# Optimization experiments

Hardware: AMD Instinct MI355X
Metric: run time of the kernel (lower is better)

## Reference

```python
import jax, jax.numpy as jnp
import numpy as np

B, S, I, H, O = 64, 512, 1024, 1024, 1024


def setup_inputs() -> dict:
    key = jax.random.key(0)
    ks = jax.random.split(key, 10)
    s = 0.02
    return {
        "x": jax.random.normal(ks[0], (B, S, I), dtype=jnp.float32),
        "W_hi": jax.random.normal(ks[1], (H, H), dtype=jnp.float32) * s,
        "W_ii": jax.random.normal(ks[2], (I, H), dtype=jnp.float32) * s,
        "W_hf": jax.random.normal(ks[3], (H, H), dtype=jnp.float32) * s,
        "W_if": jax.random.normal(ks[4], (I, H), dtype=jnp.float32) * s,
        "W_ho": jax.random.normal(ks[5], (H, H), dtype=jnp.float32) * s,
        "W_io": jax.random.normal(ks[6], (I, H), dtype=jnp.float32) * s,
        "W_hg": jax.random.normal(ks[7], (H, H), dtype=jnp.float32) * s,
        "W_ig": jax.random.normal(ks[8], (I, H), dtype=jnp.float32) * s,
        "W_y": jax.random.normal(ks[9], (H, O), dtype=jnp.float32) * s,
    }


def reference(x, W_hi, W_ii, W_hf, W_if, W_ho, W_io, W_hg, W_ig, W_y):
    b = x.shape[0]
    h0 = jnp.zeros((b, W_hi.shape[0]), dtype=x.dtype)
    c0 = jnp.zeros_like(h0)

    def step(carry, x_t):
        h, c = carry
        i = jax.nn.sigmoid(h @ W_hi + x_t @ W_ii)
        f = jax.nn.sigmoid(h @ W_hf + x_t @ W_if)
        o = jax.nn.sigmoid(h @ W_ho + x_t @ W_io)
        g = jnp.tanh(h @ W_hg + x_t @ W_ig)
        c = f * c + i * g
        h = o * jnp.tanh(c)
        return (h, c), None

    # scan over time: x -> [S, B, I]
    (h_T, _), _ = jax.lax.scan(step, (h0, c0), jnp.swapaxes(x, 0, 1))
    return h_T @ W_y
```

## Files before the change

### kernel.cpp

```cpp
#include <hip/hip_runtime.h>


typedef __bf16 bfv8 __attribute__((ext_vector_type(8)));
typedef float f32x4 __attribute__((ext_vector_type(4)));
typedef unsigned int u32v4 __attribute__((ext_vector_type(4)));

__device__ __forceinline__ unsigned short f2bf(float x) {
    union { float f; unsigned int u; } v; v.f = x;
    unsigned int r = (v.u + 0x7FFFu + ((v.u >> 16) & 1u)) >> 16;
    return (unsigned short)r;
}
__device__ __forceinline__ float bf2f(unsigned short s) {
    union { unsigned int u; float f; } v; v.u = ((unsigned int)s) << 16;
    return v.f;
}

struct SrcPtrs { const float* p[9]; };

#define ISSUE8(A, P, O0, O1, O2, O3, O4, O5, O6, O7)                         \
    asm volatile(                                                            \
        "global_load_dwordx4 %0, %8, off offset:" O0 " sc1\n\t"              \
        "global_load_dwordx4 %1, %8, off offset:" O1 " sc1\n\t"              \
        "global_load_dwordx4 %2, %8, off offset:" O2 " sc1\n\t"              \
        "global_load_dwordx4 %3, %8, off offset:" O3 " sc1\n\t"              \
        "global_load_dwordx4 %4, %8, off offset:" O4 " sc1\n\t"              \
        "global_load_dwordx4 %5, %8, off offset:" O5 " sc1\n\t"              \
        "global_load_dwordx4 %6, %8, off offset:" O6 " sc1\n\t"              \
        "global_load_dwordx4 %7, %8, off offset:" O7 " sc1"                  \
        : "=&v"(A[0]), "=&v"(A[1]), "=&v"(A[2]), "=&v"(A[3]),                \
          "=&v"(A[4]), "=&v"(A[5]), "=&v"(A[6]), "=&v"(A[7])                 \
        : "v"(P)                                                             \
        : "memory")

#define ISSUE8C(A, P, O0, O1, O2, O3, O4, O5, O6, O7)                        \
    asm volatile(                                                            \
        "global_load_dwordx4 %0, %8, off offset:" O0 "\n\t"                  \
        "global_load_dwordx4 %1, %8, off offset:" O1 "\n\t"                  \
        "global_load_dwordx4 %2, %8, off offset:" O2 "\n\t"                  \
        "global_load_dwordx4 %3, %8, off offset:" O3 "\n\t"                  \
        "global_load_dwordx4 %4, %8, off offset:" O4 "\n\t"                  \
        "global_load_dwordx4 %5, %8, off offset:" O5 "\n\t"                  \
        "global_load_dwordx4 %6, %8, off offset:" O6 "\n\t"                  \
        "global_load_dwordx4 %7, %8, off offset:" O7                         \
        : "=&v"(A[0]), "=&v"(A[1]), "=&v"(A[2]), "=&v"(A[3]),                \
          "=&v"(A[4]), "=&v"(A[5]), "=&v"(A[6]), "=&v"(A[7])                 \
        : "v"(P)                                                             \
        : "memory")

#define WAIT8(N, A)                                                          \
    do {                                                                     \
        asm volatile("s_waitcnt vmcnt(" N ")"                                \
                     : "+v"(A[0]), "+v"(A[1]), "+v"(A[2]), "+v"(A[3]),       \
                       "+v"(A[4]), "+v"(A[5]), "+v"(A[6]), "+v"(A[7])        \
                     :: "memory");                                           \
        __builtin_amdgcn_sched_barrier(0);                                   \
    } while (0)

#define CONSUME8(A, IT0)                                                     \
    _Pragma("unroll")                                                        \
    for (int j = 0; j < 8; ++j) {                                            \
        _Pragma("unroll")                                                    \
        for (int n = 0; n < 2; ++n) {                                        \
            const int off = (((((IT0) + j) << 1) | n) << 10) + (lane << 4);  \
            acc[n] = __builtin_amdgcn_mfma_f32_16x16x32_bf16(                \
                A[j], *(const bfv8*)(Lw + off), acc[n], 0, 0, 0);            \
        }                                                                    \
    }

#define ISSUE32(P)                                                           \
    do {                                                                     \
        ISSUE8(A0, P, "0", "64", "128", "192", "256", "320", "384", "448");  \
        ISSUE8(A1, P, "512", "576", "640", "704", "768", "832", "896", "960"); \
        ISSUE8(A2, P, "1024", "1088", "1152", "1216", "1280", "1344", "1408", "1472"); \
        ISSUE8(A3, P, "1536", "1600", "1664", "1728", "1792", "1856", "1920", "1984"); \
    } while (0)

#define CHKMAX(A)                                                            \
    _Pragma("unroll")                                                        \
    for (int j = 0; j < 8; ++j) {                                            \
        const u32v4 u = __builtin_bit_cast(u32v4, A[j]);                     \
        mh = mh > u.x ? mh : u.x;                                            \
        mh = mh > u.y ? mh : u.y;                                            \
        mh = mh > u.z ? mh : u.z;                                            \
        mh = mh > u.w ? mh : u.w;                                            \
    }

__global__ __launch_bounds__(256) void pack_weights(SrcPtrs sp,
                                                    unsigned short* __restrict__ Whp,
                                                    unsigned short* __restrict__ Wip,
                                                    unsigned short* __restrict__ Wy) {
    __shared__ float tile[64][65];
    const int z = blockIdx.z;
    const float* __restrict__ src = sp.p[z];
    const int n0 = blockIdx.x * 64, k0 = blockIdx.y * 64;
    const int tc = threadIdx.x & 63, tq = threadIdx.x >> 6;

    #pragma unroll
    for (int r = 0; r < 16; ++r) {
        const int kk = tq * 16 + r;
        tile[kk][tc] = src[(size_t)(k0 + kk) * 1024 + n0 + tc];
    }
    __syncthreads();
    #pragma unroll
    for (int r = 0; r < 16; ++r) {
        const int nl = tq * 16 + r;
        const int n = n0 + nl;
        const int k = k0 + tc;
        const unsigned short v = f2bf(tile[tc][nl]);
        if (z < 8) {
            const int g = z & 3;
            const int blk = n >> 3;
            const int c = (g << 3) | (n & 7);
            const int lanef = (c & 15) | (((k >> 3) & 3) << 4);
            const size_t off = ((size_t)((((blk << 5) | (k >> 5)) << 1) | (c >> 4)) << 9)
                             + (lanef << 3) + (k & 7);
            (z < 4 ? Whp : Wip)[off] = v;
        } else {
            Wy[(size_t)n * 1024 + k] = v;
        }
    }
}

__global__ __launch_bounds__(256) void convert_x(const float* __restrict__ x,
                                                 unsigned short* __restrict__ xT) {
    const size_t gid = (size_t)blockIdx.x * 256 + threadIdx.x;
    const int i0 = (int)(gid & 255) * 4;
    const size_t row = gid >> 8;
    const int t = (int)(row >> 6), b = (int)(row & 63);
    const float4 v = *reinterpret_cast<const float4*>(x + (((size_t)b * 512 + t) << 10) + i0);
    ushort4 o;
    o.x = f2bf(v.x); o.y = f2bf(v.y); o.z = f2bf(v.z); o.w = f2bf(v.w);
    *reinterpret_cast<ushort4*>(xT + (row << 10) + i0) = o;
}

__global__ __launch_bounds__(256) void lstm_pc(const unsigned short* __restrict__ xT,
                                               const unsigned short* __restrict__ Whp,
                                               const unsigned short* __restrict__ Wip,
                                               unsigned short* __restrict__ hring,
                                               int* __restrict__ xflg,
                                               int* __restrict__ cflg,
                                               int* __restrict__ flg,
                                               unsigned short* __restrict__ ring) {
    __shared__ struct {
        __align__(16) unsigned char wp[65536];
        __align__(16) unsigned char pad[32768];
        __align__(16) unsigned short hs[64][8];
    } L;
    unsigned char* Lw = L.wp;

    const int tid = threadIdx.x;
    const int w = tid >> 6;
    const int lane = tid & 63;
    const int lr = lane & 15;
    const int kq = lane >> 4;
    const bool isFactory = (blockIdx.x >= 128);
    const int b = isFactory ? (blockIdx.x - 128) : blockIdx.x;

    {
        const unsigned short* src = (isFactory ? Wip : Whp) + ((size_t)b << 15);
        #pragma unroll
        for (int s = 0; s < 16; ++s) {
            const int c = s * 256 + tid;
            *(bfv8*)(L.wp + c * 16) = *(const bfv8*)(src + c * 8);
        }
    }
    __syncthreads();

    const int roff = ((w << 4) + lr) * 1024 + kq * 8;
    const int pw = (b << 2) + w;

    if (isFactory) {
        for (int tt = 0; tt < 512; ++tt) {
            const int* cfp = cflg + pw * 32;
            while (__hip_atomic_load(cfp, __ATOMIC_RELAXED, __HIP_MEMORY_SCOPE_AGENT) < tt - 4)
                __builtin_amdgcn_s_sleep(2);

            const unsigned short* Axp = xT + ((size_t)tt << 16) + roff;
            f32x4 acc[2] = {};
            bfv8 A0[8], A1[8];
            ISSUE8C(A0, Axp, "0", "64", "128", "192", "256", "320", "384", "448");
            ISSUE8C(A1, Axp, "512", "576", "640", "704", "768", "832", "896", "960");
            WAIT8("8", A0);
            CONSUME8(A0, 0);
            ISSUE8C(A0, Axp, "1024", "1088", "1152", "1216", "1280", "1344", "1408", "1472");
            WAIT8("8", A1);
            CONSUME8(A1, 8);
            ISSUE8C(A1, Axp, "1536", "1600", "1664", "1728", "1792", "1856", "1920", "1984");
            WAIT8("8", A0);
            CONSUME8(A0, 16);
            WAIT8("0", A1);
            CONSUME8(A1, 24);

            unsigned short vv[8];
            #pragma unroll
            for (int n = 0; n < 2; ++n)
                #pragma unroll
                for (int r = 0; r < 4; ++r)
                    vv[n * 4 + r] = f2bf(acc[n][r]);
            unsigned short* rp = ring + (((size_t)(b << 2) + (tt & 3)) * 4 + w) * 512 + lane * 8;
            asm volatile("global_store_dwordx4 %0, %1, off sc1"
                         :: "v"(rp), "v"(*(const u32v4*)vv) : "memory");
            asm volatile("s_waitcnt vmcnt(0)" ::: "memory");
            if (lane == 0)
                asm volatile("global_store_dword %0, %1, off sc1"
                             :: "v"(xflg + pw * 32), "v"(tt + 1) : "memory");
        }
        return;
    }

    float cst[4] = {0.f, 0.f, 0.f, 0.f};
    bfv8 A0[8], A1[8], A2[8], A3[8];
    const u32v4 PZ = {0xFFFFFFFFu, 0xFFFFFFFFu, 0xFFFFFFFFu, 0xFFFFFFFFu};

    for (int t = 0; t < 512; ++t) {
        const unsigned short* hp = hring + ((size_t)(t & 15) << 16) + roff;

        const int* xfp = xflg + pw * 32;
        while (__hip_atomic_load(xfp, __ATOMIC_RELAXED, __HIP_MEMORY_SCOPE_AGENT) < t + 1)
            __builtin_amdgcn_s_sleep(1);
        u32v4 xp;
        const unsigned short* rp = ring + (((size_t)(b << 2) + (t & 3)) * 4 + w) * 512 + lane * 8;
        asm volatile("global_load_dwordx4 %0, %1, off sc1"
                     : "=v"(xp) : "v"(rp) : "memory");

        #define POLLG(G)                                                      \
            if (t > 0) {                                                      \
                const int* fp = flg + (((((G) << 5) + (lane & 31)) << 2) | w) * 32; \
                for (;;) {                                                    \
                    const int f = __hip_atomic_load(fp, __ATOMIC_RELAXED,     \
                                                    __HIP_MEMORY_SCOPE_AGENT);\
                    if (__all(f >= t)) break;                                 \
                    __builtin_amdgcn_s_sleep(1);                              \
                }                                                             \
            }
        POLLG(0) ISSUE8(A0, hp, "0", "64", "128", "192", "256", "320", "384", "448");
        POLLG(1) ISSUE8(A1, hp, "512", "576", "640", "704", "768", "832", "896", "960");
        POLLG(2) ISSUE8(A2, hp, "1024", "1088", "1152", "1216", "1280", "1344", "1408", "1472");
        POLLG(3) ISSUE8(A3, hp, "1536", "1600", "1664", "1728", "1792", "1856", "1920", "1984");
        #undef POLLG

        int guard = 0;
        for (;;) {
            WAIT8("0", A0); WAIT8("0", A1); WAIT8("0", A2); WAIT8("0", A3);
            asm volatile("s_waitcnt vmcnt(0)" : "+v"(xp) :: "memory");
            __builtin_amdgcn_sched_barrier(0);
            unsigned mh = 0;
            CHKMAX(A0) CHKMAX(A1) CHKMAX(A2) CHKMAX(A3)
            if (!__any(mh == 0xFFFFFFFFu) || ++guard > 65536) break;
            ISSUE32(hp);
        }

        if (lane == 0)
            asm volatile("global_store_dword %0, %1, off sc1"
                         :: "v"(cflg + pw * 32), "v"(t) : "memory");

        if (t >= 1 && lane < 16) {
            unsigned short* pz = hring + ((size_t)((t - 1) & 15) << 16)
                               + (size_t)w * 16384 + (size_t)b * 128;
            asm volatile("global_store_dwordx4 %0, %1, off sc1"
                         :: "v"(pz + lane * 8), "v"(PZ) : "memory");
        }

        f32x4 acc[2] = {};
        CONSUME8(A0, 0);
        CONSUME8(A1, 8);
        CONSUME8(A2, 16);
        CONSUME8(A3, 24);

        {
            const unsigned d0 = xp.x, d1 = xp.y, d2 = xp.z, d3 = xp.w;
            acc[0][0] += bf2f((unsigned short)(d0 & 0xFFFFu));
            acc[0][1] += bf2f((unsigned short)(d0 >> 16));
            acc[0][2] += bf2f((unsigned short)(d1 & 0xFFFFu));
            acc[0][3] += bf2f((unsigned short)(d1 >> 16));
            acc[1][0] += bf2f((unsigned short)(d2 & 0xFFFFu));
            acc[1][1] += bf2f((unsigned short)(d2 >> 16));
            acc[1][2] += bf2f((unsigned short)(d3 & 0xFFFFu));
            acc[1][3] += bf2f((unsigned short)(d3 >> 16));
        }

        const bool low = (lr & 8) == 0;
        unsigned short hsv[4];
        #pragma unroll
        for (int r = 0; r < 4; ++r) {
            const float s0 = acc[0][r], s1 = acc[1][r];
            const float x0 = __shfl_xor(s0, 8);
            const float x1 = __shfl_xor(s1, 8);
            const float pi = low ? s0 : x0;
            const float pf = low ? x0 : s0;
            const float po = low ? s1 : x1;
            const float pg = low ? x1 : s1;
            const float ig = 1.f / (1.f + __expf(-pi));
            const float fg = 1.f / (1.f + __expf(-pf));
            const float og = 1.f / (1.f + __expf(-po));
            const float gg = 1.f - 2.f / (__expf(2.f * pg) + 1.f);
            const float cn = fg * cst[r] + ig * gg;
            cst[r] = cn;
            hsv[r] = f2bf(og * (1.f - 2.f / (__expf(2.f * cn) + 1.f)));
        }

        if (low) {
            #pragma unroll
            for (int r = 0; r < 4; ++r)
                L.hs[(w << 4) + (kq << 2) + r][lr] = hsv[r];
        }
        asm volatile("s_waitcnt lgkmcnt(0)" ::: "memory");
        __builtin_amdgcn_sched_barrier(0);
        {
            unsigned short* hout = hring + ((size_t)((t + 1) & 15) << 16);
            if (lane < 16) {
                const int row = (w << 4) + lane;
                const u32v4 hv = *reinterpret_cast<const u32v4*>(&L.hs[row][0]);
                asm volatile("global_store_dwordx4 %0, %1, off sc1"
                             :: "v"(hout + (size_t)row * 1024 + (b << 3)), "v"(hv)
                             : "memory");
            }
        }
        if (lane == 0)
            asm volatile("global_store_dword %0, %1, off sc1"
                         :: "v"(flg + (pw) * 32), "v"(t + 1) : "memory");
    }
}

__global__ __launch_bounds__(256) void final_gemm(const unsigned short* __restrict__ h_in,
                                                  const unsigned short* __restrict__ WyT,
                                                  float* __restrict__ out) {
    const int tid = threadIdx.x;
    const int w = tid >> 6;
    const int lane = tid & 63;
    const int lr = lane & 15;
    const int kq = lane >> 4;
    const int c0 = blockIdx.x * 16;
    const int k0 = w * 256;

    f32x4 acc[4] = {};
    #pragma unroll 2
    for (int it = 0; it < 8; ++it) {
        const int k = k0 + it * 32 + kq * 8;
        const bfv8 bfr = *reinterpret_cast<const bfv8*>(WyT + (size_t)(c0 + lr) * 1024 + k);
        #pragma unroll
        for (int m = 0; m < 4; ++m) {
            const bfv8 a = *reinterpret_cast<const bfv8*>(h_in + (size_t)(m * 16 + lr) * 1024 + k);
            acc[m] = __builtin_amdgcn_mfma_f32_16x16x32_bf16(a, bfr, acc[m], 0, 0, 0);
        }
    }
    __shared__ float red[4][64][17];
    #pragma unroll
    for (int m = 0; m < 4; ++m)
        #pragma unroll
        for (int r = 0; r < 4; ++r)
            red[w][m * 16 + kq * 4 + r][lr] = acc[m][r];
    __syncthreads();
    #pragma unroll
    for (int u = 0; u < 4; ++u) {
        const int item = u * 256 + tid;
        const int b = item >> 4;
        const int jr = item & 15;
        const float s = red[0][b][jr] + red[1][b][jr] + red[2][b][jr] + red[3][b][jr];
        out[b * 1024 + c0 + jr] = s;
    }
}

extern "C" void kernel_launch(void* const* d_in, const int* in_sizes, int n_in,
                              void* d_out, int out_size, void* d_ws, size_t ws_size,
                              hipStream_t stream) {
    const float* x = (const float*)d_in[0];
    SrcPtrs sp;
    sp.p[0] = (const float*)d_in[1];
    sp.p[1] = (const float*)d_in[3];
    sp.p[2] = (const float*)d_in[5];
    sp.p[3] = (const float*)d_in[7];
    sp.p[4] = (const float*)d_in[2];
    sp.p[5] = (const float*)d_in[4];
    sp.p[6] = (const float*)d_in[6];
    sp.p[7] = (const float*)d_in[8];
    sp.p[8] = (const float*)d_in[9];

    char* ws = (char*)d_ws;
    unsigned short* Whp   = (unsigned short*)(ws + 0);
    unsigned short* Wip   = (unsigned short*)(ws + 8388608);
    unsigned short* Wy    = (unsigned short*)(ws + 16777216);
    unsigned short* xT    = (unsigned short*)(ws + 18874368);
    unsigned short* hring = (unsigned short*)(ws + 85983232);
    unsigned short* ring  = (unsigned short*)(ws + 88080384);
    int*            xflg  = (int*)(ws + 90177536);
    int*            cflg  = (int*)(ws + 90243072);
    int*            flg   = (int*)(ws + 90308608);

    pack_weights<<<dim3(16, 16, 9), 256, 0, stream>>>(sp, Whp, Wip, Wy);
    convert_x<<<32768, 256, 0, stream>>>(x, xT);
    hipMemsetAsync(hring, 0xFF, 16 * 131072, stream);
    hipMemsetAsync(hring, 0x00, 131072, stream);
    hipMemsetAsync(xflg, 0x00, 65536, stream);
    hipMemsetAsync(cflg, 0xFF, 65536, stream);
    hipMemsetAsync(flg, 0x00, 65536, stream);

    lstm_pc<<<256, 256, 0, stream>>>(xT, Whp, Wip, hring, xflg, cflg, flg, ring);

    final_gemm<<<64, 256, 0, stream>>>(hring, Wy, (float*)d_out);
}
```

Measured before the change: 3.218 ms.

## Pipeline h-state loads with MFMA consumption using staged waitcnt and per-group validation

Stops waiting for all 32 hidden-state loads before any compute. Each group of 8 loads is now waited on with a partial vmcnt, validated for the sentinel, retried only for that group if needed, and consumed by MFMAs while the later groups are still in flight. The completion flag store moves to just after the first group is consumed. The retry path becomes per-group, and the vmcnt counts must match the exact issue order of the loads, including the xp load.

```diff
diff --git a/kernel.cpp b/kernel.cpp
--- a/kernel.cpp
+++ b/kernel.cpp
@@ -67,14 +67,6 @@
         }                                                                    \
     }
 
-#define ISSUE32(P)                                                           \
-    do {                                                                     \
-        ISSUE8(A0, P, "0", "64", "128", "192", "256", "320", "384", "448");  \
-        ISSUE8(A1, P, "512", "576", "640", "704", "768", "832", "896", "960"); \
-        ISSUE8(A2, P, "1024", "1088", "1152", "1216", "1280", "1344", "1408", "1472"); \
-        ISSUE8(A3, P, "1536", "1600", "1664", "1728", "1792", "1856", "1920", "1984"); \
-    } while (0)
-
 #define CHKMAX(A)                                                            \
     _Pragma("unroll")                                                        \
     for (int j = 0; j < 8; ++j) {                                            \
@@ -84,6 +76,19 @@
         mh = mh > u.z ? mh : u.z;                                            \
         mh = mh > u.w ? mh : u.w;                                            \
     }
+
+#define VALIDATE(A, O0, O1, O2, O3, O4, O5, O6, O7)                          \
+    do {                                                                     \
+        unsigned mh = 0;                                                     \
+        CHKMAX(A)                                                            \
+        int guard = 0;                                                       \
+        while (__any(mh == 0xFFFFFFFFu) && ++guard <= 65536) {               \
+            ISSUE8(A, hp, O0, O1, O2, O3, O4, O5, O6, O7);                   \
+            WAIT8("0", A);                                                   \
+            mh = 0;                                                          \
+            CHKMAX(A)                                                        \
+        }                                                                    \
+    } while (0)
 
 __global__ __launch_bounds__(256) void pack_weights(SrcPtrs sp,
                                                     unsigned short* __restrict__ Whp,
@@ -239,20 +244,23 @@
         POLLG(3) ISSUE8(A3, hp, "1536", "1600", "1664", "1728", "1792", "1856", "1920", "1984");
         #undef POLLG
 
-        int guard = 0;
-        for (;;) {
-            WAIT8("0", A0); WAIT8("0", A1); WAIT8("0", A2); WAIT8("0", A3);
-            asm volatile("s_waitcnt vmcnt(0)" : "+v"(xp) :: "memory");
-            __builtin_amdgcn_sched_barrier(0);
-            unsigned mh = 0;
-            CHKMAX(A0) CHKMAX(A1) CHKMAX(A2) CHKMAX(A3)
-            if (!__any(mh == 0xFFFFFFFFu) || ++guard > 65536) break;
-            ISSUE32(hp);
-        }
-
+        f32x4 acc[2] = {};
+        WAIT8("24", A0);
+        asm volatile("" : "+v"(xp));
+        VALIDATE(A0, "0", "64", "128", "192", "256", "320", "384", "448");
+        CONSUME8(A0, 0);
         if (lane == 0)
             asm volatile("global_store_dword %0, %1, off sc1"
                          :: "v"(cflg + pw * 32), "v"(t) : "memory");
+        WAIT8("17", A1);
+        VALIDATE(A1, "512", "576", "640", "704", "768", "832", "896", "960");
+        CONSUME8(A1, 8);
+        WAIT8("9", A2);
+        VALIDATE(A2, "1024", "1088", "1152", "1216", "1280", "1344", "1408", "1472");
+        CONSUME8(A2, 16);
+        WAIT8("1", A3);
+        VALIDATE(A3, "1536", "1600", "1664", "1728", "1792", "1856", "1920", "1984");
+        CONSUME8(A3, 24);
 
         if (t >= 1 && lane < 16) {
             unsigned short* pz = hring + ((size_t)((t - 1) & 15) << 16)
@@ -260,12 +268,6 @@
             asm volatile("global_store_dwordx4 %0, %1, off sc1"
                          :: "v"(pz + lane * 8), "v"(PZ) : "memory");
         }
-
-        f32x4 acc[2] = {};
-        CONSUME8(A0, 0);
-        CONSUME8(A1, 8);
-        CONSUME8(A2, 16);
-        CONSUME8(A3, 24);
 
         {
             const unsigned d0 = xp.x, d1 = xp.y, d2 = xp.z, d3 = xp.w;
```

Result: faster. 3.045 ms (median of 2 runs) (-5.4%).
